# Kernel tuning notes

Hardware: AMD Instinct MI355X
Metric: run time of the kernel (lower is better)

The kernel has to match this reference:

```python
import jax, jax.numpy as jnp
import numpy as np

N1, N2, N3 = 3, 5, 7
BATCH = 262144


def setup_inputs() -> dict:
    key = jax.random.key(0)
    k1, k2, k3, k4 = jax.random.split(key, 4)
    D1 = jax.random.normal(k1, (BATCH, N1, N1), dtype=jnp.float32)
    D2 = jax.random.normal(k2, (BATCH, N2, N2), dtype=jnp.float32)
    D3 = jax.random.normal(k3, (BATCH, N3, N3), dtype=jnp.float32)
    # learned Clebsch-Gordan coefficient tensor (the layer's only weight)
    cg_coeffs = jax.random.normal(k4, (N1, N2, N3), dtype=jnp.float32)
    return {"D1": D1, "D2": D2, "D3": D3, "cg_coeffs": cg_coeffs}


def reference(D1, D2, D3, cg_coeffs):
    # lhs: rotate cg by D1 (left) and D2 (middle) -> [x, n1, n2, n3]
    lhs = jnp.einsum('xai,xbj,ijc->xabc', D1, D2, cg_coeffs)
    # rhs: rotate cg by D3 on the last index -> [x, n1, n2, n3]
    rhs = jnp.einsum('abi,xic->xabc', cg_coeffs, D3)
    residual = lhs - rhs
    return jnp.mean(residual * residual)
```

## Files before the change

### kernel.cpp

```cpp
#include <hip/hip_runtime.h>

#define BDIM 256

__global__ __launch_bounds__(BDIM) void cg_main_kernel(
    const float* __restrict__ D1, const float* __restrict__ D2,
    const float* __restrict__ D3, const float* __restrict__ cg,
    float* __restrict__ partials, int batch)
{
    __shared__ float cg_s[105];
    const int tid = threadIdx.x;
    if (tid < 105) cg_s[tid] = cg[tid];
    __syncthreads();

    const int x = blockIdx.x * BDIM + tid;
    float acc = 0.0f;
    if (x < batch) {
        const float* p1 = D1 + (size_t)x * 9;
        const float* p2 = D2 + (size_t)x * 25;
        const float* p3 = D3 + (size_t)x * 49;
        float d1[9], d2[25], d3[49];
        #pragma unroll
        for (int i = 0; i < 9; ++i)  d1[i] = p1[i];
        #pragma unroll
        for (int i = 0; i < 25; ++i) d2[i] = p2[i];
        #pragma unroll
        for (int i = 0; i < 49; ++i) d3[i] = p3[i];

        #pragma unroll
        for (int a = 0; a < 3; ++a) {
            float Ua[35];
            #pragma unroll
            for (int j = 0; j < 5; ++j) {
                #pragma unroll
                for (int c = 0; c < 7; ++c) {
                    float u = d1[a*3+0] * cg_s[      j*7 + c];
                    u = fmaf(d1[a*3+1],  cg_s[35 +  j*7 + c], u);
                    u = fmaf(d1[a*3+2],  cg_s[70 +  j*7 + c], u);
                    Ua[j*7+c] = u;
                }
            }
            #pragma unroll
            for (int b = 0; b < 5; ++b) {
                float cgab[7];
                #pragma unroll
                for (int i = 0; i < 7; ++i) cgab[i] = cg_s[(a*5+b)*7 + i];
                #pragma unroll
                for (int c = 0; c < 7; ++c) {
                    float L = d2[b*5+0] * Ua[c];
                    #pragma unroll
                    for (int j = 1; j < 5; ++j) L = fmaf(d2[b*5+j], Ua[j*7+c], L);
                    float R = cgab[0] * d3[c];
                    #pragma unroll
                    for (int i = 1; i < 7; ++i) R = fmaf(cgab[i], d3[i*7+c], R);
                    const float r = L - R;
                    acc = fmaf(r, r, acc);
                }
            }
        }
    }

    #pragma unroll
    for (int off = 32; off > 0; off >>= 1)
        acc += __shfl_down(acc, off, 64);
    __shared__ float wsum[BDIM / 64];
    if ((tid & 63) == 0) wsum[tid >> 6] = acc;
    __syncthreads();
    if (tid == 0) {
        float s = 0.0f;
        #pragma unroll
        for (int w = 0; w < BDIM / 64; ++w) s += wsum[w];
        partials[blockIdx.x] = s;
    }
}

__global__ __launch_bounds__(BDIM) void cg_reduce_kernel(
    const float* __restrict__ partials, float* __restrict__ out,
    int n, float inv)
{
    const int tid = threadIdx.x;
    float s = 0.0f;
    for (int i = tid; i < n; i += BDIM) s += partials[i];
    #pragma unroll
    for (int off = 32; off > 0; off >>= 1)
        s += __shfl_down(s, off, 64);
    __shared__ float wsum[BDIM / 64];
    if ((tid & 63) == 0) wsum[tid >> 6] = s;
    __syncthreads();
    if (tid == 0) {
        float t = 0.0f;
        #pragma unroll
        for (int w = 0; w < BDIM / 64; ++w) t += wsum[w];
        out[0] = t * inv;
    }
}

extern "C" void kernel_launch(void* const* d_in, const int* in_sizes, int n_in,
                              void* d_out, int out_size, void* d_ws, size_t ws_size,
                              hipStream_t stream)
{
    const float* D1 = (const float*)d_in[0];
    const float* D2 = (const float*)d_in[1];
    const float* D3 = (const float*)d_in[2];
    const float* cg = (const float*)d_in[3];
    float* out      = (float*)d_out;
    float* partials = (float*)d_ws;

    const int batch   = in_sizes[0] / 9;
    const int nblocks = (batch + BDIM - 1) / BDIM;
    const float inv   = 1.0f / ((float)batch * 105.0f);

    cg_main_kernel<<<nblocks, BDIM, 0, stream>>>(D1, D2, D3, cg, partials, batch);
    cg_reduce_kernel<<<1, BDIM, 0, stream>>>(partials, out, nblocks, inv);
}
```

Baseline: 25.69 us.

## Stage D2/D3 through LDS with coalesced float4 loads, one wave per block

Each 64-thread block now copies its wave's contiguous D2 and D3 slices into shared memory with coalesced float4 loads, then each lane reads its own matrix from LDS instead of doing strided per-thread global loads. U is precomputed for all three rows up front, and the block-level reduction collapses to a single wave shuffle. The cost is about 19 KB of LDS per 64-thread block, which limits how many blocks fit per CU. The bounds check is also removed, so the batch is assumed to be a multiple of 64.

```diff
diff --git a/kernel.cpp b/kernel.cpp
--- a/kernel.cpp
+++ b/kernel.cpp
@@ -2,59 +2,82 @@
 
 #define BDIM 256
 
-__global__ __launch_bounds__(BDIM) void cg_main_kernel(
+__global__ __launch_bounds__(64, 2) void cg_main_kernel(
     const float* __restrict__ D1, const float* __restrict__ D2,
     const float* __restrict__ D3, const float* __restrict__ cg,
-    float* __restrict__ partials, int batch)
+    float* __restrict__ partials)
 {
-    __shared__ float cg_s[105];
-    const int tid = threadIdx.x;
-    if (tid < 105) cg_s[tid] = cg[tid];
+    __shared__ __align__(16) float s_d2[64 * 25];
+    __shared__ __align__(16) float s_d3[64 * 49];
+    __shared__ float s_cg[105];
+
+    const int lane = threadIdx.x;
+    const int w    = blockIdx.x;
+
+    for (int i = lane; i < 105; i += 64) s_cg[i] = cg[i];
+
+    const float4* g2 = (const float4*)(D2 + (size_t)w * (64 * 25));
+    float4* l2 = (float4*)s_d2;
+    #pragma unroll
+    for (int k = 0; k < 7; ++k) {
+        int idx = k * 64 + lane;
+        if (idx < 400) l2[idx] = g2[idx];
+    }
+    const float4* g3 = (const float4*)(D3 + (size_t)w * (64 * 49));
+    float4* l3 = (float4*)s_d3;
+    #pragma unroll
+    for (int k = 0; k < 13; ++k) {
+        int idx = k * 64 + lane;
+        if (idx < 784) l3[idx] = g3[idx];
+    }
     __syncthreads();
 
-    const int x = blockIdx.x * BDIM + tid;
+    const int x = w * 64 + lane;
+
+    float d1[9];
+    const float* p1 = D1 + (size_t)x * 9;
+    #pragma unroll
+    for (int i = 0; i < 9; ++i) d1[i] = p1[i];
+
+    float U[3][35];
+    #pragma unroll
+    for (int j = 0; j < 5; ++j) {
+        #pragma unroll
+        for (int c = 0; c < 7; ++c) {
+            const float c0 = s_cg[     j * 7 + c];
+            const float c1 = s_cg[35 + j * 7 + c];
+            const float c2 = s_cg[70 + j * 7 + c];
+            U[0][j * 7 + c] = fmaf(d1[2], c2, fmaf(d1[1], c1, d1[0] * c0));
+            U[1][j * 7 + c] = fmaf(d1[5], c2, fmaf(d1[4], c1, d1[3] * c0));
+            U[2][j * 7 + c] = fmaf(d1[8], c2, fmaf(d1[7], c1, d1[6] * c0));
+        }
+    }
+
+    float d2[25];
+    #pragma unroll
+    for (int j = 0; j < 25; ++j) d2[j] = s_d2[lane * 25 + j];
+    float d3[49];
+    #pragma unroll
+    for (int i = 0; i < 49; ++i) d3[i] = s_d3[lane * 49 + i];
+
     float acc = 0.0f;
-    if (x < batch) {
-        const float* p1 = D1 + (size_t)x * 9;
-        const float* p2 = D2 + (size_t)x * 25;
-        const float* p3 = D3 + (size_t)x * 49;
-        float d1[9], d2[25], d3[49];
+    #pragma unroll
+    for (int a = 0; a < 3; ++a) {
         #pragma unroll
-        for (int i = 0; i < 9; ++i)  d1[i] = p1[i];
-        #pragma unroll
-        for (int i = 0; i < 25; ++i) d2[i] = p2[i];
-        #pragma unroll
-        for (int i = 0; i < 49; ++i) d3[i] = p3[i];
-
-        #pragma unroll
-        for (int a = 0; a < 3; ++a) {
-            float Ua[35];
+        for (int b = 0; b < 5; ++b) {
+            float cgab[7];
             #pragma unroll
-            for (int j = 0; j < 5; ++j) {
+            for (int i = 0; i < 7; ++i) cgab[i] = s_cg[(a * 5 + b) * 7 + i];
+            #pragma unroll
+            for (int c = 0; c < 7; ++c) {
+                float L = d2[b * 5] * U[a][c];
                 #pragma unroll
-                for (int c = 0; c < 7; ++c) {
-                    float u = d1[a*3+0] * cg_s[      j*7 + c];
-                    u = fmaf(d1[a*3+1],  cg_s[35 +  j*7 + c], u);
-                    u = fmaf(d1[a*3+2],  cg_s[70 +  j*7 + c], u);
-                    Ua[j*7+c] = u;
-                }
-            }
-            #pragma unroll
-            for (int b = 0; b < 5; ++b) {
-                float cgab[7];
+                for (int j = 1; j < 5; ++j) L = fmaf(d2[b * 5 + j], U[a][j * 7 + c], L);
+                float R = cgab[0] * d3[c];
                 #pragma unroll
-                for (int i = 0; i < 7; ++i) cgab[i] = cg_s[(a*5+b)*7 + i];
-                #pragma unroll
-                for (int c = 0; c < 7; ++c) {
-                    float L = d2[b*5+0] * Ua[c];
-                    #pragma unroll
-                    for (int j = 1; j < 5; ++j) L = fmaf(d2[b*5+j], Ua[j*7+c], L);
-                    float R = cgab[0] * d3[c];
-                    #pragma unroll
-                    for (int i = 1; i < 7; ++i) R = fmaf(cgab[i], d3[i*7+c], R);
-                    const float r = L - R;
-                    acc = fmaf(r, r, acc);
-                }
+                for (int i = 1; i < 7; ++i) R = fmaf(cgab[i], d3[i * 7 + c], R);
+                const float r = L - R;
+                acc = fmaf(r, r, acc);
             }
         }
     }
@@ -62,15 +85,7 @@
     #pragma unroll
     for (int off = 32; off > 0; off >>= 1)
         acc += __shfl_down(acc, off, 64);
-    __shared__ float wsum[BDIM / 64];
-    if ((tid & 63) == 0) wsum[tid >> 6] = acc;
-    __syncthreads();
-    if (tid == 0) {
-        float s = 0.0f;
-        #pragma unroll
-        for (int w = 0; w < BDIM / 64; ++w) s += wsum[w];
-        partials[blockIdx.x] = s;
-    }
+    if (lane == 0) partials[w] = acc;
 }
 
 __global__ __launch_bounds__(BDIM) void cg_reduce_kernel(
@@ -105,10 +120,10 @@
     float* out      = (float*)d_out;
     float* partials = (float*)d_ws;
 
-    const int batch   = in_sizes[0] / 9;
-    const int nblocks = (batch + BDIM - 1) / BDIM;
-    const float inv   = 1.0f / ((float)batch * 105.0f);
+    const int batch  = in_sizes[0] / 9;
+    const int nwaves = batch / 64;
+    const float inv  = 1.0f / ((float)batch * 105.0f);
 
-    cg_main_kernel<<<nblocks, BDIM, 0, stream>>>(D1, D2, D3, cg, partials, batch);
-    cg_reduce_kernel<<<1, BDIM, 0, stream>>>(partials, out, nblocks, inv);
+    cg_main_kernel<<<nwaves, 64, 0, stream>>>(D1, D2, D3, cg, partials);
+    cg_reduce_kernel<<<1, BDIM, 0, stream>>>(partials, out, nwaves, inv);
 }
```

Measured after the change: 40.97 us. 59.5% more time.
